# Performance work log

Hardware: AMD Instinct MI355X
Metric: run time of the kernel (lower is better)

Reference implementation:

```python
import jax, jax.numpy as jnp
import numpy as np

B, C, H, W = 8, 3, 64, 64
HORIZON = 32
WIDTH = 32
M1 = M2 = M3 = 8
N_LAYERS = 4
C_OUT = 3


def setup_inputs() -> dict:
    key = jax.random.key(0)
    ks = jax.random.split(key, 16)
    scale = 1.0 / (WIDTH * WIDTH)
    wshape = (N_LAYERS, 4, WIDTH, WIDTH, M1, M2, M3)
    return {
        "x_t": jax.random.normal(ks[0], (B, C, H, W), dtype=jnp.float32),
        "p_w": jax.random.normal(ks[1], (WIDTH, C + 3), dtype=jnp.float32) * 0.1,
        "p_b": jnp.zeros((WIDTH,), dtype=jnp.float32),
        "spec_wr": scale * jax.random.normal(ks[2], wshape, dtype=jnp.float32),
        "spec_wi": scale * jax.random.normal(ks[3], wshape, dtype=jnp.float32),
        "pw_w": jax.random.normal(ks[4], (N_LAYERS, WIDTH, WIDTH), dtype=jnp.float32) * 0.1,
        "pw_b": jnp.zeros((N_LAYERS, WIDTH), dtype=jnp.float32),
        "q1_w": jax.random.normal(ks[5], (2 * WIDTH, WIDTH), dtype=jnp.float32) * 0.1,
        "q1_b": jnp.zeros((2 * WIDTH,), dtype=jnp.float32),
        "q2_w": jax.random.normal(ks[6], (C_OUT, 2 * WIDTH), dtype=jnp.float32) * 0.1,
        "q2_b": jnp.zeros((C_OUT,), dtype=jnp.float32),
        "horizon": HORIZON,
    }


def _conv1x1(x, w, b):
    # x: [b, i, x, y, z], w: [o, i] -> [b, o, x, y, z]
    return jnp.einsum("oi,bixyz->boxyz", w, x) + b[None, :, None, None, None]


def _spectral_conv3d(x, wr, wi):
    # x: [b, i, H, W, T]; wr/wi: [4, i, o, m1, m2, m3]
    h, w_, t = x.shape[-3], x.shape[-2], x.shape[-1]
    xf = jnp.fft.rfftn(x, axes=(-3, -2, -1))  # [b, i, H, W, T//2+1]
    wc = (wr + 1j * wi).astype(xf.dtype)
    m1 = min(M1, xf.shape[-3]); m2 = min(M2, xf.shape[-2]); m3 = min(M3, xf.shape[-1])
    mul = lambda a, ww: jnp.einsum("bixyz,ioxyz->boxyz", a, ww)
    out = jnp.zeros((x.shape[0], wr.shape[2]) + xf.shape[2:], dtype=xf.dtype)
    out = out.at[:, :, :m1, :m2, :m3].set(mul(xf[:, :, :m1, :m2, :m3], wc[0, :, :, :m1, :m2, :m3]))
    out = out.at[:, :, -m1:, :m2, :m3].set(mul(xf[:, :, -m1:, :m2, :m3], wc[1, :, :, :m1, :m2, :m3]))
    out = out.at[:, :, :m1, -m2:, :m3].set(mul(xf[:, :, :m1, -m2:, :m3], wc[2, :, :, :m1, :m2, :m3]))
    out = out.at[:, :, -m1:, -m2:, :m3].set(mul(xf[:, :, -m1:, -m2:, :m3], wc[3, :, :, :m1, :m2, :m3]))
    return jnp.fft.irfftn(out, s=(h, w_, t), axes=(-3, -2, -1))


def _grid_3d(b, h, w, t, dtype):
    gy = jnp.broadcast_to(jnp.linspace(0.0, 1.0, h, dtype=dtype)[None, None, :, None, None], (b, 1, h, w, t))
    gx = jnp.broadcast_to(jnp.linspace(0.0, 1.0, w, dtype=dtype)[None, None, None, :, None], (b, 1, h, w, t))
    gt = jnp.broadcast_to(jnp.linspace(0.0, 1.0, t, dtype=dtype)[None, None, None, None, :], (b, 1, h, w, t))
    return jnp.concatenate([gy, gx, gt], axis=1)


def reference(x_t, p_w, p_b, spec_wr, spec_wi, pw_w, pw_b, q1_w, q1_b, q2_w, q2_b, horizon):
    b, c, h, w = x_t.shape
    x = jnp.broadcast_to(x_t[..., None], (b, c, h, w, horizon))  # repeat over time
    grid = _grid_3d(b, h, w, horizon, x_t.dtype)
    x = jnp.concatenate([x, grid], axis=1)  # [b, c+3, h, w, t]
    x = _conv1x1(x, p_w, p_b)
    for l in range(N_LAYERS):
        x = jax.nn.gelu(
            _spectral_conv3d(x, spec_wr[l], spec_wi[l]) + _conv1x1(x, pw_w[l], pw_b[l]),
            approximate=False,
        )
    x = _conv1x1(x, q1_w, q1_b)
    x = jax.nn.gelu(x, approximate=False)
    x = _conv1x1(x, q2_w, q2_b)
    # [b, c_out, h, w, t] -> [b, t, c_out, h, w]
    return jnp.transpose(x, (0, 4, 1, 2, 3))
```

## Files before the change

### kernel.cpp

```cpp
#include <hip/hip_runtime.h>
#include <math.h>


#define TWO_PI 6.2831853071795864769f

typedef short bf16x8 __attribute__((ext_vector_type(8)));
typedef float f32x4 __attribute__((ext_vector_type(4)));
typedef float v2f __attribute__((ext_vector_type(2)));

__device__ __forceinline__ f32x4 mfma16(bf16x8 a, bf16x8 b, f32x4 c) {
    return __builtin_amdgcn_mfma_f32_16x16x32_bf16(a, b, c, 0, 0, 0);
}

__device__ __forceinline__ void split8(float4 a, float4 b, bf16x8& h, bf16x8& l) {
    float f[8] = {a.x, a.y, a.z, a.w, b.x, b.y, b.z, b.w};
    #pragma unroll
    for (int i = 0; i < 8; ++i) {
        unsigned u = __float_as_uint(f[i]);
        h[i] = (short)(u >> 16);
        float hf = __uint_as_float(u & 0xFFFF0000u);
        float lf = f[i] - hf;
        l[i] = (short)(__float_as_uint(lf) >> 16);
    }
}

__device__ __forceinline__ unsigned packhl(float f) {
    unsigned u = __float_as_uint(f);
    unsigned hi = u & 0xFFFF0000u;
    float lf = f - __uint_as_float(hi);
    return hi | (__float_as_uint(lf) >> 16);
}

__device__ __forceinline__ void unpack8(uint4 a, uint4 b, bf16x8& h, bf16x8& l) {
    unsigned u[8] = {a.x, a.y, a.z, a.w, b.x, b.y, b.z, b.w};
    #pragma unroll
    for (int i = 0; i < 8; ++i) {
        h[i] = (short)(u[i] >> 16);
        l[i] = (short)(u[i] & 0xFFFFu);
    }
}

__device__ __forceinline__ v2f make2(float x) { v2f r; r.x = x; r.y = x; return r; }
__device__ __forceinline__ v2f fma2(v2f a, v2f b, v2f c) { return __builtin_elementwise_fma(a, b, c); }

__device__ __forceinline__ v2f gelu2(v2f v) {
    v2f u = v * 0.70710678118654752f;
    v2f a = __builtin_elementwise_abs(u);
    v2f den = fma2(a, make2(0.3275911f), make2(1.0f));
    v2f t; t.x = __builtin_amdgcn_rcpf(den.x); t.y = __builtin_amdgcn_rcpf(den.y);
    v2f p = t * (0.254829592f + t * (-0.284496736f + t * (1.421413741f +
            t * (-1.453152027f + t * 1.061405429f))));
    v2f e; e.x = __expf(-u.x * u.x); e.y = __expf(-u.y * u.y);
    v2f m = fma2(-p, e, make2(1.0f));
    v2f erfu = __builtin_elementwise_copysign(m, u);
    return 0.5f * v * (1.0f + erfu);
}

__device__ __forceinline__ void gelu4(f32x4& q) {
    v2f p0; p0.x = q[0]; p0.y = q[1];
    v2f p1; p1.x = q[2]; p1.y = q[3];
    p0 = gelu2(p0); p1 = gelu2(p1);
    q[0] = p0.x; q[1] = p0.y; q[2] = p1.x; q[3] = p1.y;
}

__device__ __forceinline__ void make_fwd_A(int l15, int quad, bf16x8& Gh, bf16x8& Gl) {
    int k = l15 >> 1;
    float s0, c0, ds, dc;
    __sincosf((float)(k * quad * 8) * (TWO_PI / 32.0f), &s0, &c0);
    __sincosf((float)k * (TWO_PI / 32.0f), &ds, &dc);
    float m[8];
    float cc = c0, ss = s0;
    #pragma unroll
    for (int j = 0; j < 8; ++j) {
        m[j] = (l15 & 1) ? -ss : cc;
        float nc = cc * dc - ss * ds;
        float ns = ss * dc + cc * ds;
        cc = nc; ss = ns;
    }
    split8(make_float4(m[0], m[1], m[2], m[3]),
           make_float4(m[4], m[5], m[6], m[7]), Gh, Gl);
}

__device__ __forceinline__ void fwd_tdft(const unsigned* up, int b, int sp0,
                                         float2* __restrict__ T1,
                                         int wb, int l15, int quad,
                                         bf16x8 Gh, bf16x8 Gl) {
    #pragma unroll
    for (int nt = 0; nt < 4; ++nt) {
        int r = wb + nt * 16 + l15;
        const uint4* p = (const uint4*)(up + r * 36 + quad * 8);
        bf16x8 bh, bl; unpack8(p[0], p[1], bh, bl);
        f32x4 d = {0.f, 0.f, 0.f, 0.f};
        d = mfma16(Gh, bh, d);
        d = mfma16(Gl, bh, d);
        d = mfma16(Gh, bl, d);
        int c = r & 31, spl = r >> 5;
        float4* ob = (float4*)(T1 + ((long)(b * 32 + c) * 4096 + sp0 + spl) * 8 + quad * 2);
        *ob = make_float4(d[0], d[1], d[2], d[3]);
    }
}

__device__ __forceinline__ void make_invx_A(int x0, int l15, int quad, bf16x8& Ah, bf16x8& Al) {
    int spl = l15 >> 1, ro = l15 & 1;
    float xx = (float)(x0 + spl);
    const float S = 1.0f / 131072.0f;
    float f[8];
    #pragma unroll
    for (int m = 0; m < 4; ++m) {
        int kxi = quad * 4 + m;
        float kx = (float)(kxi < 8 ? kxi : kxi - 16);
        float sn, cs;
        __sincosf(kx * xx * (TWO_PI / 64.0f), &sn, &cs);
        f[2 * m]     = ro ? S * sn : S * cs;
        f[2 * m + 1] = ro ? S * cs : -S * sn;
    }
    split8(make_float4(f[0], f[1], f[2], f[3]),
           make_float4(f[4], f[5], f[6], f[7]), Ah, Al);
}

__device__ __forceinline__ void stage_T5_half(const float2* __restrict__ T5, float* smem,
                                              int b, int y, int half, int tid) {
    float2* T5h = (float2*)(smem + 4224);
    int c = tid >> 4, q4 = tid & 15;
    const float4* src = (const float4*)(T5 + ((long)((b * 32 + half * 16 + c) * 64 + y)) * 128);
    float4* dst = (float4*)(T5h + c * 130);
    #pragma unroll
    for (int j = 0; j < 4; ++j) dst[q4 + j * 16] = src[q4 + j * 16];
}

__device__ __forceinline__ void invx_half(float* smem, int half, int wave, int l15, int quad,
                                          bf16x8 xAh, bf16x8 xAl) {
    const float2* T5h = (const float2*)(smem + 4224);
    #pragma unroll
    for (int nt2 = 0; nt2 < 2; ++nt2) {
        int tile = wave * 2 + nt2;
        int ol = tile * 2 + (l15 >> 3), kt = l15 & 7;
        float f[8];
        #pragma unroll
        for (int m = 0; m < 4; ++m) {
            float2 v = T5h[ol * 130 + (quad * 4 + m) * 8 + kt];
            f[2 * m] = v.x; f[2 * m + 1] = v.y;
        }
        bf16x8 bh, bl;
        split8(make_float4(f[0], f[1], f[2], f[3]),
               make_float4(f[4], f[5], f[6], f[7]), bh, bl);
        f32x4 d = {0.f, 0.f, 0.f, 0.f};
        d = mfma16(xAh, bh, d);
        d = mfma16(xAl, bh, d);
        d = mfma16(xAh, bl, d);
        int o = half * 16 + ol;
        #pragma unroll
        for (int reg = 0; reg < 4; ++reg) {
            int m_ = quad * 4 + reg, spl = m_ >> 1, ri = m_ & 1;
            smem[o * 132 + spl * 16 + kt * 2 + ri] = d[reg];
        }
    }
}

__global__ __launch_bounds__(256) void k_lift(const float* __restrict__ xt,
                                              const float* __restrict__ pw,
                                              const float* __restrict__ pb,
                                              unsigned* __restrict__ X,
                                              float2* __restrict__ T1) {
    __shared__ unsigned xs[9216];
    int gg = blockIdx.x;
    int g = ((gg & 7) << 9) | (gg >> 3);
    int spt = g & 511, b = g >> 9;
    int sp0 = spt * 8;
    int y = sp0 >> 6, x0 = sp0 & 63;
    int tid = threadIdx.x;
    int t = tid & 31, spl = tid >> 5;
    int sp = sp0 + spl;
    float a0 = xt[(b * 3 + 0) * 4096 + sp];
    float a1 = xt[(b * 3 + 1) * 4096 + sp];
    float a2 = xt[(b * 3 + 2) * 4096 + sp];
    float gy = y * (1.0f / 63.0f), gx = (x0 + spl) * (1.0f / 63.0f), gt = t * (1.0f / 31.0f);
    float v[32];
    #pragma unroll
    for (int c = 0; c < 32; ++c) {
        const float* w = pw + c * 6;
        v[c] = pb[c] + w[0] * a0 + w[1] * a1 + w[2] * a2
             + w[3] * gy + w[4] * gx + w[5] * gt;
    }
    unsigned pk[32];
    #pragma unroll
    for (int c = 0; c < 32; ++c) pk[c] = packhl(v[c]);
    unsigned* xg = X + (((long)(b * 4096 + sp)) * 32 + t) * 32;
    #pragma unroll
    for (int j = 0; j < 8; ++j)
        ((uint4*)xg)[j] = make_uint4(pk[4*j], pk[4*j+1], pk[4*j+2], pk[4*j+3]);
    #pragma unroll
    for (int c = 0; c < 32; ++c)
        xs[(spl * 32 + c) * 36 + t] = pk[c];
    int wave = tid >> 6, lane = tid & 63, l15 = lane & 15, quad = lane >> 4;
    bf16x8 Gh, Gl; make_fwd_A(l15, quad, Gh, Gl);
    __syncthreads();
    fwd_tdft(xs, b, sp0, T1, wave * 64, l15, quad, Gh, Gl);
}

__global__ __launch_bounds__(256) void k_xdft(const float2* __restrict__ T1, float2* __restrict__ T2) {
    __shared__ float2 s[1024];
    __shared__ float2 tw[64];
    int g = blockIdx.x;
    int ypair = g & 31; int bc = g >> 5;
    long base = ((long)bc * 64 + ypair * 2) * 512;
    int tid = threadIdx.x;
    for (int k = tid; k < 1024; k += 256) s[k] = T1[base + k];
    if (tid < 64) { float sn, cs; __sincosf(tid * (TWO_PI / 64.0f), &sn, &cs); tw[tid] = make_float2(cs, sn); }
    __syncthreads();
    #pragma unroll
    for (int r = 0; r < 2; ++r) {
        int j = tid + r * 256;
        int half = j >> 8, rem = j & 255;
        int idx = half * 512 + rem;
        float2 a = s[idx], b2 = s[idx + 256];
        s[idx] = make_float2(a.x + b2.x, a.y + b2.y);
        s[idx + 256] = make_float2(a.x - b2.x, a.y - b2.y);
    }
    __syncthreads();
    int half = tid >> 7, jj = tid & 127;
    int kxi = jj >> 3, kt = jj & 7;
    int kx = kxi < 8 ? kxi : kxi + 48;
    const float2* row = s + half * 512 + (kx & 1) * 256;
    float sr = 0.f, si = 0.f;
    for (int x = 0; x < 32; ++x) {
        float2 w = tw[(kx * x) & 63];
        float2 a = row[x * 8 + kt];
        sr += a.x * w.x + a.y * w.y;
        si += a.y * w.x - a.x * w.y;
    }
    T2[((long)bc * 64 + ypair * 2 + half) * 128 + jj] = make_float2(sr, si);
}

__global__ __launch_bounds__(128) void k_ydft(const float2* __restrict__ T2, float2* __restrict__ T3) {
    __shared__ float2 s[512];
    __shared__ float2 tw[64];
    int g = blockIdx.x;
    int kx = g & 15; int bc = g >> 4;
    int tid = threadIdx.x;
    for (int k = tid; k < 512; k += 128) {
        int y = k >> 3, kt = k & 7;
        s[k] = T2[((long)bc * 64 + y) * 128 + kx * 8 + kt];
    }
    if (tid < 64) { float sn, cs; __sincosf(tid * (TWO_PI / 64.0f), &sn, &cs); tw[tid] = make_float2(cs, sn); }
    __syncthreads();
    #pragma unroll
    for (int r = 0; r < 2; ++r) {
        int j = tid + r * 128;
        float2 a = s[j], b2 = s[j + 256];
        s[j] = make_float2(a.x + b2.x, a.y + b2.y);
        s[j + 256] = make_float2(a.x - b2.x, a.y - b2.y);
    }
    __syncthreads();
    int kyi = tid >> 3, kt = tid & 7;
    int ky = kyi < 8 ? kyi : kyi + 48;
    const float2* row = s + (ky & 1) * 256;
    float sr = 0.f, si = 0.f;
    for (int y = 0; y < 32; ++y) {
        float2 w = tw[(ky * y) & 63];
        float2 a = row[y * 8 + kt];
        sr += a.x * w.x + a.y * w.y;
        si += a.y * w.x - a.x * w.y;
    }
    T3[((long)bc * 256 + kyi * 16 + kx) * 8 + kt] = make_float2(sr, si);
}

__global__ __launch_bounds__(256) void k_mix2(const float2* __restrict__ T3,
                                              const float* __restrict__ wr,
                                              const float* __restrict__ wi,
                                              float2* __restrict__ T4, int layer) {
    __shared__ float2 s[2304];
    int mode = blockIdx.x;
    int kyi = mode >> 4, kxi = mode & 15;
    int tid = threadIdx.x;
    {
        int bb = tid >> 5, i = tid & 31;
        const float2* src = T3 + ((long)(bb * 32 + i) * 256 + mode) * 8;
        float2* dst = s + (i * 8 + bb) * 9;
        #pragma unroll
        for (int k = 0; k < 8; ++k) dst[k] = src[k];
    }
    __syncthreads();
    int corner = (kyi >= 8 ? 1 : 0) + (kxi >= 8 ? 2 : 0);
    long wbase = (long)(layer * 4 + corner) * 524288 + (long)(kyi & 7) * 64 + (long)(kxi & 7) * 8;
    int o = tid >> 3, kt = tid & 7;
    long wb = wbase + (long)o * 512 + kt;
    float2 acc[8];
    #pragma unroll
    for (int bb = 0; bb < 8; ++bb) acc[bb] = make_float2(0.f, 0.f);
    for (int i = 0; i < 32; ++i) {
        float r = wr[wb + (long)i * 16384], im = wi[wb + (long)i * 16384];
        #pragma unroll
        for (int bb = 0; bb < 8; ++bb) {
            float2 a = s[(i * 8 + bb) * 9 + kt];
            acc[bb].x += a.x * r - a.y * im;
            acc[bb].y += a.x * im + a.y * r;
        }
    }
    #pragma unroll
    for (int bb = 0; bb < 8; ++bb)
        T4[((long)(bb * 32 + o) * 256 + mode) * 8 + kt] = acc[bb];
}

__global__ __launch_bounds__(256) void k_invy(const float2* __restrict__ T4, float2* __restrict__ T5) {
    __shared__ float2 s[128];
    __shared__ float2 tw[64];
    __shared__ float2 pmP[56], pmM[56];
    int g = blockIdx.x;
    int kx = g & 15; int bc = g >> 4;
    int tid = threadIdx.x;
    if (tid < 128) {
        int kyi = tid >> 3, kt = tid & 7;
        s[tid] = T4[((long)bc * 256 + kyi * 16 + kx) * 8 + kt];
    } else if (tid < 192) {
        int m = tid - 128; float sn, cs; __sincosf(m * (TWO_PI / 64.0f), &sn, &cs); tw[m] = make_float2(cs, sn);
    }
    __syncthreads();
    if (tid < 56) {
        int j = (tid >> 3) + 1, kt = tid & 7;
        float2 a = s[j * 8 + kt], b2 = s[(16 - j) * 8 + kt];
        pmP[tid] = make_float2(a.x + b2.x, a.y + b2.y);
        pmM[tid] = make_float2(a.x - b2.x, a.y - b2.y);
    }
    __syncthreads();
    #pragma unroll
    for (int r = 0; r < 2; ++r) {
        int j = tid + r * 256;
        int y = j >> 3, kt = j & 7;
        float2 A0 = s[kt], A8 = s[64 + kt];
        float2 w8 = tw[(8 * y) & 63];
        float sr = A0.x + A8.x * w8.x + A8.y * w8.y;
        float si = A0.y + A8.y * w8.x - A8.x * w8.y;
        #pragma unroll
        for (int jj = 1; jj < 8; ++jj) {
            float2 w = tw[(jj * y) & 63];
            float2 P = pmP[(jj - 1) * 8 + kt], M = pmM[(jj - 1) * 8 + kt];
            sr += P.x * w.x - M.y * w.y;
            si += P.y * w.x + M.x * w.y;
        }
        T5[((long)bc * 64 + y) * 128 + kx * 8 + kt] = make_float2(sr, si);
    }
}

__device__ __forceinline__ void make_invt_A(int l15, int quad, bf16x8 Ah[2], bf16x8 Al[2]) {
    #pragma unroll
    for (int th = 0; th < 2; ++th) {
        float m[8];
        if (quad < 2) {
            int tt = th * 16 + l15;
            #pragma unroll
            for (int kk = 0; kk < 4; ++kk) {
                int k = quad * 4 + kk;
                float sn, cs;
                __sincosf((float)(k * tt) * (TWO_PI / 32.0f), &sn, &cs);
                float w = k ? 2.0f : 1.0f;
                m[2 * kk] = w * cs;
                m[2 * kk + 1] = -w * sn;
            }
        } else {
            #pragma unroll
            for (int j = 0; j < 8; ++j) m[j] = 0.f;
        }
        split8(make_float4(m[0], m[1], m[2], m[3]),
               make_float4(m[4], m[5], m[6], m[7]), Ah[th], Al[th]);
    }
}

__global__ __launch_bounds__(256) void k_fuse3(unsigned* __restrict__ X, const float2* __restrict__ T5,
                                               const float* __restrict__ pww,
                                               const float* __restrict__ pwb,
                                               float2* __restrict__ T1, int layer) {
    __shared__ float smem[9216];
    int gg = blockIdx.x;
    int g = ((gg & 7) << 9) | (gg >> 3);
    int spt = g & 511, b = g >> 9;
    int sp0 = spt * 8;
    int y = sp0 >> 6, x0 = sp0 & 63;
    int tid = threadIdx.x;
    int wave = tid >> 6, lane = tid & 63, l15 = lane & 15, quad = lane >> 4;
    int wb = wave * 64;
    stage_T5_half(T5, smem, b, y, 0, tid);
    const float* wl = pww + layer * 1024;
    const float* bl = pwb + layer * 32;
    bf16x8 wah[2], wal[2];
    f32x4 acc[2][4];
    #pragma unroll
    for (int mt = 0; mt < 2; ++mt) {
        const float4* p = (const float4*)(wl + (mt * 16 + l15) * 32 + quad * 8);
        split8(p[0], p[1], wah[mt], wal[mt]);
        float4 bv = *(const float4*)(bl + mt * 16 + quad * 4);
        f32x4 bi; bi[0] = bv.x; bi[1] = bv.y; bi[2] = bv.z; bi[3] = bv.w;
        #pragma unroll
        for (int nt = 0; nt < 4; ++nt) acc[mt][nt] = bi;
    }
    #pragma unroll
    for (int nt = 0; nt < 4; ++nt) {
        int pt = wb + nt * 16 + l15;
        int spl = pt >> 5, t = pt & 31;
        const uint4* xp = (const uint4*)(X + (((long)(b * 4096 + sp0 + spl)) * 32 + t) * 32 + quad * 8);
        bf16x8 bh, blo; unpack8(xp[0], xp[1], bh, blo);
        #pragma unroll
        for (int mt = 0; mt < 2; ++mt) {
            acc[mt][nt] = mfma16(wah[mt], bh, acc[mt][nt]);
            acc[mt][nt] = mfma16(wal[mt], bh, acc[mt][nt]);
            acc[mt][nt] = mfma16(wah[mt], blo, acc[mt][nt]);
        }
    }
    bf16x8 Ah[2], Al[2];
    make_invt_A(l15, quad, Ah, Al);
    bf16x8 xAh, xAl;
    make_invx_A(x0, l15, quad, xAh, xAl);
    __syncthreads();
    invx_half(smem, 0, wave, l15, quad, xAh, xAl);
    __syncthreads();
    stage_T5_half(T5, smem, b, y, 1, tid);
    __syncthreads();
    invx_half(smem, 1, wave, l15, quad, xAh, xAl);
    __syncthreads();
    float2* ts = (float2*)smem;
    bf16x8 Bh[2][2], Bl[2][2];
    #pragma unroll
    for (int sph = 0; sph < 2; ++sph) {
        int spl = 2 * wave + sph;
        #pragma unroll
        for (int ch = 0; ch < 2; ++ch) {
            float4 q0 = make_float4(0.f, 0.f, 0.f, 0.f), q1 = q0;
            if (quad < 2) {
                const float4* p = (const float4*)(ts + (ch * 16 + l15) * 66 + spl * 8 + quad * 4);
                q0 = p[0]; q1 = p[1];
            }
            split8(q0, q1, Bh[sph][ch], Bl[sph][ch]);
        }
    }
    __syncthreads();
    #pragma unroll
    for (int sph = 0; sph < 2; ++sph)
        #pragma unroll
        for (int ch = 0; ch < 2; ++ch)
            #pragma unroll
            for (int th = 0; th < 2; ++th) {
                int nt = sph * 2 + th;
                acc[ch][nt] = mfma16(Bh[sph][ch], Ah[th], acc[ch][nt]);
                acc[ch][nt] = mfma16(Bl[sph][ch], Ah[th], acc[ch][nt]);
                acc[ch][nt] = mfma16(Bh[sph][ch], Al[th], acc[ch][nt]);
            }
    bf16x8 Gh, Gl; make_fwd_A(l15, quad, Gh, Gl);
    #pragma unroll
    for (int mt = 0; mt < 2; ++mt)
        #pragma unroll
        for (int nt = 0; nt < 4; ++nt) gelu4(acc[mt][nt]);
    unsigned* up = (unsigned*)smem;
    #pragma unroll
    for (int mt = 0; mt < 2; ++mt)
        #pragma unroll
        for (int nt = 0; nt < 4; ++nt) {
            int pt = wb + nt * 16 + l15;
            int spl = pt >> 5, t = pt & 31;
            int o0 = mt * 16 + quad * 4;
            unsigned pk0 = packhl(acc[mt][nt][0]), pk1 = packhl(acc[mt][nt][1]);
            unsigned pk2 = packhl(acc[mt][nt][2]), pk3 = packhl(acc[mt][nt][3]);
            *(uint4*)(X + (((long)(b * 4096 + sp0 + spl)) * 32 + t) * 32 + o0) =
                make_uint4(pk0, pk1, pk2, pk3);
            up[(spl * 32 + o0 + 0) * 36 + t] = pk0;
            up[(spl * 32 + o0 + 1) * 36 + t] = pk1;
            up[(spl * 32 + o0 + 2) * 36 + t] = pk2;
            up[(spl * 32 + o0 + 3) * 36 + t] = pk3;
        }
    __syncthreads();
    fwd_tdft(up, b, sp0, T1, wb, l15, quad, Gh, Gl);
}

__global__ __launch_bounds__(256) void k_fuse3_last(const unsigned* __restrict__ X, const float2* __restrict__ T5,
                                                    const float* __restrict__ pww, const float* __restrict__ pwb,
                                                    const float* __restrict__ q1w, const float* __restrict__ q1b,
                                                    const float* __restrict__ q2w, const float* __restrict__ q2b,
                                                    float* __restrict__ out) {
    __shared__ float smem[9408];
    int gg = blockIdx.x;
    int g = ((gg & 7) << 9) | (gg >> 3);
    int spt = g & 511, b = g >> 9;
    int sp0 = spt * 8;
    int y = sp0 >> 6, x0 = sp0 & 63;
    int tid = threadIdx.x;
    int wave = tid >> 6, lane = tid & 63, l15 = lane & 15, quad = lane >> 4;
    int wb = wave * 64;
    stage_T5_half(T5, smem, b, y, 0, tid);
    if (tid < 192) smem[9216 + tid] = q2w[tid];
    const float* wl = pww + 3 * 1024;
    const float* bl = pwb + 3 * 32;
    bf16x8 wah[2], wal[2];
    f32x4 acc[2][4];
    #pragma unroll
    for (int mt = 0; mt < 2; ++mt) {
        const float4* p = (const float4*)(wl + (mt * 16 + l15) * 32 + quad * 8);
        split8(p[0], p[1], wah[mt], wal[mt]);
        float4 bv = *(const float4*)(bl + mt * 16 + quad * 4);
        f32x4 bi; bi[0] = bv.x; bi[1] = bv.y; bi[2] = bv.z; bi[3] = bv.w;
        #pragma unroll
        for (int nt = 0; nt < 4; ++nt) acc[mt][nt] = bi;
    }
    #pragma unroll
    for (int nt = 0; nt < 4; ++nt) {
        int pt = wb + nt * 16 + l15;
        int spl = pt >> 5, t = pt & 31;
        const uint4* xp = (const uint4*)(X + (((long)(b * 4096 + sp0 + spl)) * 32 + t) * 32 + quad * 8);
        bf16x8 bh, blo; unpack8(xp[0], xp[1], bh, blo);
        #pragma unroll
        for (int mt = 0; mt < 2; ++mt) {
            acc[mt][nt] = mfma16(wah[mt], bh, acc[mt][nt]);
            acc[mt][nt] = mfma16(wal[mt], bh, acc[mt][nt]);
            acc[mt][nt] = mfma16(wah[mt], blo, acc[mt][nt]);
        }
    }
    bf16x8 Ah[2], Al[2];
    make_invt_A(l15, quad, Ah, Al);
    bf16x8 xAh, xAl;
    make_invx_A(x0, l15, quad, xAh, xAl);
    __syncthreads();
    invx_half(smem, 0, wave, l15, quad, xAh, xAl);
    __syncthreads();
    stage_T5_half(T5, smem, b, y, 1, tid);
    __syncthreads();
    invx_half(smem, 1, wave, l15, quad, xAh, xAl);
    __syncthreads();
    float2* ts = (float2*)smem;
    bf16x8 Bh[2][2], Bl[2][2];
    #pragma unroll
    for (int sph = 0; sph < 2; ++sph) {
        int spl = 2 * wave + sph;
        #pragma unroll
        for (int ch = 0; ch < 2; ++ch) {
            float4 q0 = make_float4(0.f, 0.f, 0.f, 0.f), q1 = q0;
            if (quad < 2) {
                const float4* p = (const float4*)(ts + (ch * 16 + l15) * 66 + spl * 8 + quad * 4);
                q0 = p[0]; q1 = p[1];
            }
            split8(q0, q1, Bh[sph][ch], Bl[sph][ch]);
        }
    }
    __syncthreads();
    #pragma unroll
    for (int sph = 0; sph < 2; ++sph)
        #pragma unroll
        for (int ch = 0; ch < 2; ++ch)
            #pragma unroll
            for (int th = 0; th < 2; ++th) {
                int nt = sph * 2 + th;
                acc[ch][nt] = mfma16(Bh[sph][ch], Ah[th], acc[ch][nt]);
                acc[ch][nt] = mfma16(Bl[sph][ch], Ah[th], acc[ch][nt]);
                acc[ch][nt] = mfma16(Bh[sph][ch], Al[th], acc[ch][nt]);
            }
    #pragma unroll
    for (int mt = 0; mt < 2; ++mt)
        #pragma unroll
        for (int nt = 0; nt < 4; ++nt) gelu4(acc[mt][nt]);
    unsigned* up = (unsigned*)smem;
    #pragma unroll
    for (int mt = 0; mt < 2; ++mt)
        #pragma unroll
        for (int nt = 0; nt < 4; ++nt) {
            int pt = wb + nt * 16 + l15;
            int o0 = mt * 16 + quad * 4;
            *(uint4*)(up + pt * 36 + o0) =
                make_uint4(packhl(acc[mt][nt][0]), packhl(acc[mt][nt][1]),
                           packhl(acc[mt][nt][2]), packhl(acc[mt][nt][3]));
        }
    __syncthreads();
    bf16x8 qah[4], qal[4];
    f32x4 qbv[4];
    #pragma unroll
    for (int mt = 0; mt < 4; ++mt) {
        const float4* p = (const float4*)(q1w + (mt * 16 + l15) * 32 + quad * 8);
        split8(p[0], p[1], qah[mt], qal[mt]);
        float4 bv = *(const float4*)(q1b + mt * 16 + quad * 4);
        qbv[mt][0] = bv.x; qbv[mt][1] = bv.y; qbv[mt][2] = bv.z; qbv[mt][3] = bv.w;
    }
    const float* q2l = smem + 9216;
    float q2b0 = q2b[0], q2b1 = q2b[1], q2b2 = q2b[2];
    float oc0[4], oc1[4], oc2[4];
    #pragma unroll
    for (int nt = 0; nt < 4; ++nt) {
        int pt = wb + nt * 16 + l15;
        const uint4* bp = (const uint4*)(up + pt * 36 + quad * 8);
        bf16x8 bh, blo; unpack8(bp[0], bp[1], bh, blo);
        float p0 = 0.f, p1 = 0.f, p2 = 0.f;
        #pragma unroll
        for (int mt = 0; mt < 4; ++mt) {
            f32x4 h = qbv[mt];
            h = mfma16(qah[mt], bh, h);
            h = mfma16(qal[mt], bh, h);
            h = mfma16(qah[mt], blo, h);
            gelu4(h);
            #pragma unroll
            for (int reg = 0; reg < 4; ++reg) {
                int hh = mt * 16 + quad * 4 + reg;
                p0 += q2l[hh] * h[reg];
                p1 += q2l[64 + hh] * h[reg];
                p2 += q2l[128 + hh] * h[reg];
            }
        }
        p0 += __shfl_xor(p0, 16); p0 += __shfl_xor(p0, 32);
        p1 += __shfl_xor(p1, 16); p1 += __shfl_xor(p1, 32);
        p2 += __shfl_xor(p2, 16); p2 += __shfl_xor(p2, 32);
        oc0[nt] = p0 + q2b0; oc1[nt] = p1 + q2b1; oc2[nt] = p2 + q2b2;
    }
    __syncthreads();
    if (quad == 0) {
        #pragma unroll
        for (int nt = 0; nt < 4; ++nt) {
            int pt = wb + nt * 16 + l15;
            int spl = pt >> 5, t = pt & 31;
            smem[(t * 3 + 0) * 9 + spl] = oc0[nt];
            smem[(t * 3 + 1) * 9 + spl] = oc1[nt];
            smem[(t * 3 + 2) * 9 + spl] = oc2[nt];
        }
    }
    __syncthreads();
    for (int m = tid; m < 768; m += 256) {
        int u = m >> 3, spl = m & 7;
        out[((long)(b * 96 + u)) * 4096 + sp0 + spl] = smem[u * 9 + spl];
    }
}

extern "C" void kernel_launch(void* const* d_in, const int* in_sizes, int n_in,
                              void* d_out, int out_size, void* d_ws, size_t ws_size,
                              hipStream_t stream) {
    const float* xt  = (const float*)d_in[0];
    const float* pw  = (const float*)d_in[1];
    const float* pb  = (const float*)d_in[2];
    const float* swr = (const float*)d_in[3];
    const float* swi = (const float*)d_in[4];
    const float* pww = (const float*)d_in[5];
    const float* pwb = (const float*)d_in[6];
    const float* q1w = (const float*)d_in[7];
    const float* q1b = (const float*)d_in[8];
    const float* q2w = (const float*)d_in[9];
    const float* q2b = (const float*)d_in[10];
    float* out = (float*)d_out;

    unsigned* X  = (unsigned*)d_ws;
    float2* T1 = (float2*)((float*)d_ws + 33554432);
    float2* T2 = (float2*)((float*)T1 + 16777216);
    float2* T3 = (float2*)((float*)T2 + 4194304);
    float2* T4 = (float2*)((float*)T3 + 1048576);

    k_lift<<<4096, 256, 0, stream>>>(xt, pw, pb, X, T1);
    for (int l = 0; l < 4; ++l) {
        k_xdft<<<8192, 256, 0, stream>>>(T1, T2);
        k_ydft<<<4096, 128, 0, stream>>>(T2, T3);
        k_mix2<<<256, 256, 0, stream>>>(T3, swr, swi, T4, l);
        k_invy<<<4096, 256, 0, stream>>>(T4, T2);
        if (l < 3)
            k_fuse3<<<4096, 256, 0, stream>>>(X, T2, pww, pwb, T1, l);
        else
            k_fuse3_last<<<4096, 256, 0, stream>>>(X, T2, pww, pwb, q1w, q1b, q2w, q2b, out);
    }
}
```

Before: 720.7 us.

## Precompute DFT fragment tables once, store packed bf16 splits in LDS, mix in place

Adds a one-block init kernel that builds the inverse-time, forward-time and inverse-x DFT matrix fragments (pre-split into bf16 hi/lo) into a workspace table. The lift and fuse kernels then load these instead of recomputing them with sincos per block. The inverse-x result is also written to LDS already packed as hi/lo bf16, so the later read only unpacks it and skips a second split. k_mix2 appears to write its output back into T3 instead of a separate T4, dropping one buffer. The cost is an extra launch plus global table loads, and the in-place mix is only safe if each block reads its own slice before writing.

Measured after the change: 762.9 us. +5.9%, slower.

```diff
diff --git a/kernel.cpp b/kernel.cpp
--- a/kernel.cpp
+++ b/kernel.cpp
@@ -81,25 +81,6 @@
            make_float4(m[4], m[5], m[6], m[7]), Gh, Gl);
 }
 
-__device__ __forceinline__ void fwd_tdft(const unsigned* up, int b, int sp0,
-                                         float2* __restrict__ T1,
-                                         int wb, int l15, int quad,
-                                         bf16x8 Gh, bf16x8 Gl) {
-    #pragma unroll
-    for (int nt = 0; nt < 4; ++nt) {
-        int r = wb + nt * 16 + l15;
-        const uint4* p = (const uint4*)(up + r * 36 + quad * 8);
-        bf16x8 bh, bl; unpack8(p[0], p[1], bh, bl);
-        f32x4 d = {0.f, 0.f, 0.f, 0.f};
-        d = mfma16(Gh, bh, d);
-        d = mfma16(Gl, bh, d);
-        d = mfma16(Gh, bl, d);
-        int c = r & 31, spl = r >> 5;
-        float4* ob = (float4*)(T1 + ((long)(b * 32 + c) * 4096 + sp0 + spl) * 8 + quad * 2);
-        *ob = make_float4(d[0], d[1], d[2], d[3]);
-    }
-}
-
 __device__ __forceinline__ void make_invx_A(int x0, int l15, int quad, bf16x8& Ah, bf16x8& Al) {
     int spl = l15 >> 1, ro = l15 & 1;
     float xx = (float)(x0 + spl);
@@ -116,230 +97,6 @@
     }
     split8(make_float4(f[0], f[1], f[2], f[3]),
            make_float4(f[4], f[5], f[6], f[7]), Ah, Al);
-}
-
-__device__ __forceinline__ void stage_T5_half(const float2* __restrict__ T5, float* smem,
-                                              int b, int y, int half, int tid) {
-    float2* T5h = (float2*)(smem + 4224);
-    int c = tid >> 4, q4 = tid & 15;
-    const float4* src = (const float4*)(T5 + ((long)((b * 32 + half * 16 + c) * 64 + y)) * 128);
-    float4* dst = (float4*)(T5h + c * 130);
-    #pragma unroll
-    for (int j = 0; j < 4; ++j) dst[q4 + j * 16] = src[q4 + j * 16];
-}
-
-__device__ __forceinline__ void invx_half(float* smem, int half, int wave, int l15, int quad,
-                                          bf16x8 xAh, bf16x8 xAl) {
-    const float2* T5h = (const float2*)(smem + 4224);
-    #pragma unroll
-    for (int nt2 = 0; nt2 < 2; ++nt2) {
-        int tile = wave * 2 + nt2;
-        int ol = tile * 2 + (l15 >> 3), kt = l15 & 7;
-        float f[8];
-        #pragma unroll
-        for (int m = 0; m < 4; ++m) {
-            float2 v = T5h[ol * 130 + (quad * 4 + m) * 8 + kt];
-            f[2 * m] = v.x; f[2 * m + 1] = v.y;
-        }
-        bf16x8 bh, bl;
-        split8(make_float4(f[0], f[1], f[2], f[3]),
-               make_float4(f[4], f[5], f[6], f[7]), bh, bl);
-        f32x4 d = {0.f, 0.f, 0.f, 0.f};
-        d = mfma16(xAh, bh, d);
-        d = mfma16(xAl, bh, d);
-        d = mfma16(xAh, bl, d);
-        int o = half * 16 + ol;
-        #pragma unroll
-        for (int reg = 0; reg < 4; ++reg) {
-            int m_ = quad * 4 + reg, spl = m_ >> 1, ri = m_ & 1;
-            smem[o * 132 + spl * 16 + kt * 2 + ri] = d[reg];
-        }
-    }
-}
-
-__global__ __launch_bounds__(256) void k_lift(const float* __restrict__ xt,
-                                              const float* __restrict__ pw,
-                                              const float* __restrict__ pb,
-                                              unsigned* __restrict__ X,
-                                              float2* __restrict__ T1) {
-    __shared__ unsigned xs[9216];
-    int gg = blockIdx.x;
-    int g = ((gg & 7) << 9) | (gg >> 3);
-    int spt = g & 511, b = g >> 9;
-    int sp0 = spt * 8;
-    int y = sp0 >> 6, x0 = sp0 & 63;
-    int tid = threadIdx.x;
-    int t = tid & 31, spl = tid >> 5;
-    int sp = sp0 + spl;
-    float a0 = xt[(b * 3 + 0) * 4096 + sp];
-    float a1 = xt[(b * 3 + 1) * 4096 + sp];
-    float a2 = xt[(b * 3 + 2) * 4096 + sp];
-    float gy = y * (1.0f / 63.0f), gx = (x0 + spl) * (1.0f / 63.0f), gt = t * (1.0f / 31.0f);
-    float v[32];
-    #pragma unroll
-    for (int c = 0; c < 32; ++c) {
-        const float* w = pw + c * 6;
-        v[c] = pb[c] + w[0] * a0 + w[1] * a1 + w[2] * a2
-             + w[3] * gy + w[4] * gx + w[5] * gt;
-    }
-    unsigned pk[32];
-    #pragma unroll
-    for (int c = 0; c < 32; ++c) pk[c] = packhl(v[c]);
-    unsigned* xg = X + (((long)(b * 4096 + sp)) * 32 + t) * 32;
-    #pragma unroll
-    for (int j = 0; j < 8; ++j)
-        ((uint4*)xg)[j] = make_uint4(pk[4*j], pk[4*j+1], pk[4*j+2], pk[4*j+3]);
-    #pragma unroll
-    for (int c = 0; c < 32; ++c)
-        xs[(spl * 32 + c) * 36 + t] = pk[c];
-    int wave = tid >> 6, lane = tid & 63, l15 = lane & 15, quad = lane >> 4;
-    bf16x8 Gh, Gl; make_fwd_A(l15, quad, Gh, Gl);
-    __syncthreads();
-    fwd_tdft(xs, b, sp0, T1, wave * 64, l15, quad, Gh, Gl);
-}
-
-__global__ __launch_bounds__(256) void k_xdft(const float2* __restrict__ T1, float2* __restrict__ T2) {
-    __shared__ float2 s[1024];
-    __shared__ float2 tw[64];
-    int g = blockIdx.x;
-    int ypair = g & 31; int bc = g >> 5;
-    long base = ((long)bc * 64 + ypair * 2) * 512;
-    int tid = threadIdx.x;
-    for (int k = tid; k < 1024; k += 256) s[k] = T1[base + k];
-    if (tid < 64) { float sn, cs; __sincosf(tid * (TWO_PI / 64.0f), &sn, &cs); tw[tid] = make_float2(cs, sn); }
-    __syncthreads();
-    #pragma unroll
-    for (int r = 0; r < 2; ++r) {
-        int j = tid + r * 256;
-        int half = j >> 8, rem = j & 255;
-        int idx = half * 512 + rem;
-        float2 a = s[idx], b2 = s[idx + 256];
-        s[idx] = make_float2(a.x + b2.x, a.y + b2.y);
-        s[idx + 256] = make_float2(a.x - b2.x, a.y - b2.y);
-    }
-    __syncthreads();
-    int half = tid >> 7, jj = tid & 127;
-    int kxi = jj >> 3, kt = jj & 7;
-    int kx = kxi < 8 ? kxi : kxi + 48;
-    const float2* row = s + half * 512 + (kx & 1) * 256;
-    float sr = 0.f, si = 0.f;
-    for (int x = 0; x < 32; ++x) {
-        float2 w = tw[(kx * x) & 63];
-        float2 a = row[x * 8 + kt];
-        sr += a.x * w.x + a.y * w.y;
-        si += a.y * w.x - a.x * w.y;
-    }
-    T2[((long)bc * 64 + ypair * 2 + half) * 128 + jj] = make_float2(sr, si);
-}
-
-__global__ __launch_bounds__(128) void k_ydft(const float2* __restrict__ T2, float2* __restrict__ T3) {
-    __shared__ float2 s[512];
-    __shared__ float2 tw[64];
-    int g = blockIdx.x;
-    int kx = g & 15; int bc = g >> 4;
-    int tid = threadIdx.x;
-    for (int k = tid; k < 512; k += 128) {
-        int y = k >> 3, kt = k & 7;
-        s[k] = T2[((long)bc * 64 + y) * 128 + kx * 8 + kt];
-    }
-    if (tid < 64) { float sn, cs; __sincosf(tid * (TWO_PI / 64.0f), &sn, &cs); tw[tid] = make_float2(cs, sn); }
-    __syncthreads();
-    #pragma unroll
-    for (int r = 0; r < 2; ++r) {
-        int j = tid + r * 128;
-        float2 a = s[j], b2 = s[j + 256];
-        s[j] = make_float2(a.x + b2.x, a.y + b2.y);
-        s[j + 256] = make_float2(a.x - b2.x, a.y - b2.y);
-    }
-    __syncthreads();
-    int kyi = tid >> 3, kt = tid & 7;
-    int ky = kyi < 8 ? kyi : kyi + 48;
-    const float2* row = s + (ky & 1) * 256;
-    float sr = 0.f, si = 0.f;
-    for (int y = 0; y < 32; ++y) {
-        float2 w = tw[(ky * y) & 63];
-        float2 a = row[y * 8 + kt];
-        sr += a.x * w.x + a.y * w.y;
-        si += a.y * w.x - a.x * w.y;
-    }
-    T3[((long)bc * 256 + kyi * 16 + kx) * 8 + kt] = make_float2(sr, si);
-}
-
-__global__ __launch_bounds__(256) void k_mix2(const float2* __restrict__ T3,
-                                              const float* __restrict__ wr,
-                                              const float* __restrict__ wi,
-                                              float2* __restrict__ T4, int layer) {
-    __shared__ float2 s[2304];
-    int mode = blockIdx.x;
-    int kyi = mode >> 4, kxi = mode & 15;
-    int tid = threadIdx.x;
-    {
-        int bb = tid >> 5, i = tid & 31;
-        const float2* src = T3 + ((long)(bb * 32 + i) * 256 + mode) * 8;
-        float2* dst = s + (i * 8 + bb) * 9;
-        #pragma unroll
-        for (int k = 0; k < 8; ++k) dst[k] = src[k];
-    }
-    __syncthreads();
-    int corner = (kyi >= 8 ? 1 : 0) + (kxi >= 8 ? 2 : 0);
-    long wbase = (long)(layer * 4 + corner) * 524288 + (long)(kyi & 7) * 64 + (long)(kxi & 7) * 8;
-    int o = tid >> 3, kt = tid & 7;
-    long wb = wbase + (long)o * 512 + kt;
-    float2 acc[8];
-    #pragma unroll
-    for (int bb = 0; bb < 8; ++bb) acc[bb] = make_float2(0.f, 0.f);
-    for (int i = 0; i < 32; ++i) {
-        float r = wr[wb + (long)i * 16384], im = wi[wb + (long)i * 16384];
-        #pragma unroll
-        for (int bb = 0; bb < 8; ++bb) {
-            float2 a = s[(i * 8 + bb) * 9 + kt];
-            acc[bb].x += a.x * r - a.y * im;
-            acc[bb].y += a.x * im + a.y * r;
-        }
-    }
-    #pragma unroll
-    for (int bb = 0; bb < 8; ++bb)
-        T4[((long)(bb * 32 + o) * 256 + mode) * 8 + kt] = acc[bb];
-}
-
-__global__ __launch_bounds__(256) void k_invy(const float2* __restrict__ T4, float2* __restrict__ T5) {
-    __shared__ float2 s[128];
-    __shared__ float2 tw[64];
-    __shared__ float2 pmP[56], pmM[56];
-    int g = blockIdx.x;
-    int kx = g & 15; int bc = g >> 4;
-    int tid = threadIdx.x;
-    if (tid < 128) {
-        int kyi = tid >> 3, kt = tid & 7;
-        s[tid] = T4[((long)bc * 256 + kyi * 16 + kx) * 8 + kt];
-    } else if (tid < 192) {
-        int m = tid - 128; float sn, cs; __sincosf(m * (TWO_PI / 64.0f), &sn, &cs); tw[m] = make_float2(cs, sn);
-    }
-    __syncthreads();
-    if (tid < 56) {
-        int j = (tid >> 3) + 1, kt = tid & 7;
-        float2 a = s[j * 8 + kt], b2 = s[(16 - j) * 8 + kt];
-        pmP[tid] = make_float2(a.x + b2.x, a.y + b2.y);
-        pmM[tid] = make_float2(a.x - b2.x, a.y - b2.y);
-    }
-    __syncthreads();
-    #pragma unroll
-    for (int r = 0; r < 2; ++r) {
-        int j = tid + r * 256;
-        int y = j >> 3, kt = j & 7;
-        float2 A0 = s[kt], A8 = s[64 + kt];
-        float2 w8 = tw[(8 * y) & 63];
-        float sr = A0.x + A8.x * w8.x + A8.y * w8.y;
-        float si = A0.y + A8.y * w8.x - A8.x * w8.y;
-        #pragma unroll
-        for (int jj = 1; jj < 8; ++jj) {
-            float2 w = tw[(jj * y) & 63];
-            float2 P = pmP[(jj - 1) * 8 + kt], M = pmM[(jj - 1) * 8 + kt];
-            sr += P.x * w.x - M.y * w.y;
-            si += P.y * w.x + M.x * w.y;
-        }
-        T5[((long)bc * 64 + y) * 128 + kx * 8 + kt] = make_float2(sr, si);
-    }
 }
 
 __device__ __forceinline__ void make_invt_A(int l15, int quad, bf16x8 Ah[2], bf16x8 Al[2]) {
@@ -366,10 +123,296 @@
     }
 }
 
+__device__ __forceinline__ unsigned packfrag(short h, short l) {
+    return ((unsigned)(unsigned short)h << 16) | (unsigned)(unsigned short)l;
+}
+
+__global__ __launch_bounds__(512) void k_init(unsigned* __restrict__ tabs) {
+    int tid = threadIdx.x;
+    int lane = tid & 63, xg = tid >> 6;
+    int l15 = lane & 15, quad = lane >> 4;
+    if (tid < 64) {
+        bf16x8 Ah[2], Al[2];
+        make_invt_A(l15, quad, Ah, Al);
+        #pragma unroll
+        for (int th = 0; th < 2; ++th)
+            #pragma unroll
+            for (int i = 0; i < 8; ++i)
+                tabs[lane * 16 + th * 8 + i] = packfrag(Ah[th][i], Al[th][i]);
+        bf16x8 Gh, Gl;
+        make_fwd_A(l15, quad, Gh, Gl);
+        #pragma unroll
+        for (int i = 0; i < 8; ++i)
+            tabs[1024 + lane * 8 + i] = packfrag(Gh[i], Gl[i]);
+    }
+    bf16x8 xAh, xAl;
+    make_invx_A(xg * 8, l15, quad, xAh, xAl);
+    #pragma unroll
+    for (int i = 0; i < 8; ++i)
+        tabs[1536 + xg * 512 + lane * 8 + i] = packfrag(xAh[i], xAl[i]);
+}
+
+__device__ __forceinline__ void load_invt(const uint4* tb, int lane, bf16x8 Ah[2], bf16x8 Al[2]) {
+    unpack8(tb[lane * 4 + 0], tb[lane * 4 + 1], Ah[0], Al[0]);
+    unpack8(tb[lane * 4 + 2], tb[lane * 4 + 3], Ah[1], Al[1]);
+}
+__device__ __forceinline__ void load_fwd(const uint4* tb, int lane, bf16x8& Gh, bf16x8& Gl) {
+    unpack8(tb[256 + lane * 2], tb[256 + lane * 2 + 1], Gh, Gl);
+}
+__device__ __forceinline__ void load_invx(const uint4* tb, int xg, int lane, bf16x8& Ah, bf16x8& Al) {
+    unpack8(tb[384 + (xg * 64 + lane) * 2], tb[384 + (xg * 64 + lane) * 2 + 1], Ah, Al);
+}
+
+__device__ __forceinline__ void fwd_tdft(const unsigned* up, int b, int sp0,
+                                         float2* __restrict__ T1,
+                                         int wb, int l15, int quad,
+                                         bf16x8 Gh, bf16x8 Gl) {
+    #pragma unroll
+    for (int nt = 0; nt < 4; ++nt) {
+        int r = wb + nt * 16 + l15;
+        const uint4* p = (const uint4*)(up + r * 36 + quad * 8);
+        bf16x8 bh, bl; unpack8(p[0], p[1], bh, bl);
+        f32x4 d = {0.f, 0.f, 0.f, 0.f};
+        d = mfma16(Gh, bh, d);
+        d = mfma16(Gl, bh, d);
+        d = mfma16(Gh, bl, d);
+        int c = r & 31, spl = r >> 5;
+        float4* ob = (float4*)(T1 + ((long)(b * 32 + c) * 4096 + sp0 + spl) * 8 + quad * 2);
+        *ob = make_float4(d[0], d[1], d[2], d[3]);
+    }
+}
+
+__device__ __forceinline__ void stage_T5_half(const float2* __restrict__ T5, float* smem,
+                                              int b, int y, int half, int tid) {
+    float2* T5h = (float2*)(smem + 4224);
+    int c = tid >> 4, q4 = tid & 15;
+    const float4* src = (const float4*)(T5 + ((long)((b * 32 + half * 16 + c) * 64 + y)) * 128);
+    float4* dst = (float4*)(T5h + c * 130);
+    #pragma unroll
+    for (int j = 0; j < 4; ++j) dst[q4 + j * 16] = src[q4 + j * 16];
+}
+
+__device__ __forceinline__ void invx_half(float* smem, int half, int wave, int l15, int quad,
+                                          bf16x8 xAh, bf16x8 xAl) {
+    const float2* T5h = (const float2*)(smem + 4224);
+    unsigned* tsu = (unsigned*)smem;
+    #pragma unroll
+    for (int nt2 = 0; nt2 < 2; ++nt2) {
+        int tile = wave * 2 + nt2;
+        int ol = tile * 2 + (l15 >> 3), kt = l15 & 7;
+        float f[8];
+        #pragma unroll
+        for (int m = 0; m < 4; ++m) {
+            float2 v = T5h[ol * 130 + (quad * 4 + m) * 8 + kt];
+            f[2 * m] = v.x; f[2 * m + 1] = v.y;
+        }
+        bf16x8 bh, bl;
+        split8(make_float4(f[0], f[1], f[2], f[3]),
+               make_float4(f[4], f[5], f[6], f[7]), bh, bl);
+        f32x4 d = {0.f, 0.f, 0.f, 0.f};
+        d = mfma16(xAh, bh, d);
+        d = mfma16(xAl, bh, d);
+        d = mfma16(xAh, bl, d);
+        int o = half * 16 + ol;
+        #pragma unroll
+        for (int reg = 0; reg < 4; ++reg) {
+            int m_ = quad * 4 + reg, spl = m_ >> 1, ri = m_ & 1;
+            tsu[o * 132 + spl * 16 + kt * 2 + ri] = packhl(d[reg]);
+        }
+    }
+}
+
+__global__ __launch_bounds__(256) void k_lift(const float* __restrict__ xt,
+                                              const float* __restrict__ pw,
+                                              const float* __restrict__ pb,
+                                              unsigned* __restrict__ X,
+                                              float2* __restrict__ T1,
+                                              const unsigned* __restrict__ tabs) {
+    __shared__ unsigned xs[9216];
+    int gg = blockIdx.x;
+    int g = ((gg & 7) << 9) | (gg >> 3);
+    int spt = g & 511, b = g >> 9;
+    int sp0 = spt * 8;
+    int y = sp0 >> 6, x0 = sp0 & 63;
+    int tid = threadIdx.x;
+    int t = tid & 31, spl = tid >> 5;
+    int sp = sp0 + spl;
+    float a0 = xt[(b * 3 + 0) * 4096 + sp];
+    float a1 = xt[(b * 3 + 1) * 4096 + sp];
+    float a2 = xt[(b * 3 + 2) * 4096 + sp];
+    float gy = y * (1.0f / 63.0f), gx = (x0 + spl) * (1.0f / 63.0f), gt = t * (1.0f / 31.0f);
+    float v[32];
+    #pragma unroll
+    for (int c = 0; c < 32; ++c) {
+        const float* w = pw + c * 6;
+        v[c] = pb[c] + w[0] * a0 + w[1] * a1 + w[2] * a2
+             + w[3] * gy + w[4] * gx + w[5] * gt;
+    }
+    unsigned pk[32];
+    #pragma unroll
+    for (int c = 0; c < 32; ++c) pk[c] = packhl(v[c]);
+    unsigned* xg2 = X + (((long)(b * 4096 + sp)) * 32 + t) * 32;
+    #pragma unroll
+    for (int j = 0; j < 8; ++j)
+        ((uint4*)xg2)[j] = make_uint4(pk[4*j], pk[4*j+1], pk[4*j+2], pk[4*j+3]);
+    #pragma unroll
+    for (int c = 0; c < 32; ++c)
+        xs[(spl * 32 + c) * 36 + t] = pk[c];
+    int wave = tid >> 6, lane = tid & 63, l15 = lane & 15, quad = lane >> 4;
+    bf16x8 Gh, Gl; load_fwd((const uint4*)tabs, lane, Gh, Gl);
+    __syncthreads();
+    fwd_tdft(xs, b, sp0, T1, wave * 64, l15, quad, Gh, Gl);
+}
+
+__global__ __launch_bounds__(256) void k_xdft(const float2* __restrict__ T1, float2* __restrict__ T2) {
+    __shared__ float2 s[1024];
+    __shared__ float2 tw[64];
+    int g = blockIdx.x;
+    int ypair = g & 31; int bc = g >> 5;
+    long base = ((long)bc * 64 + ypair * 2) * 512;
+    int tid = threadIdx.x;
+    for (int k = tid; k < 1024; k += 256) s[k] = T1[base + k];
+    if (tid < 64) { float sn, cs; __sincosf(tid * (TWO_PI / 64.0f), &sn, &cs); tw[tid] = make_float2(cs, sn); }
+    __syncthreads();
+    #pragma unroll
+    for (int r = 0; r < 2; ++r) {
+        int j = tid + r * 256;
+        int half = j >> 8, rem = j & 255;
+        int idx = half * 512 + rem;
+        float2 a = s[idx], b2 = s[idx + 256];
+        s[idx] = make_float2(a.x + b2.x, a.y + b2.y);
+        s[idx + 256] = make_float2(a.x - b2.x, a.y - b2.y);
+    }
+    __syncthreads();
+    int half = tid >> 7, jj = tid & 127;
+    int kxi = jj >> 3, kt = jj & 7;
+    int kx = kxi < 8 ? kxi : kxi + 48;
+    const float2* row = s + half * 512 + (kx & 1) * 256;
+    float sr = 0.f, si = 0.f;
+    for (int x = 0; x < 32; ++x) {
+        float2 w = tw[(kx * x) & 63];
+        float2 a = row[x * 8 + kt];
+        sr += a.x * w.x + a.y * w.y;
+        si += a.y * w.x - a.x * w.y;
+    }
+    T2[((long)bc * 64 + ypair * 2 + half) * 128 + jj] = make_float2(sr, si);
+}
+
+__global__ __launch_bounds__(128) void k_ydft(const float2* __restrict__ T2, float2* __restrict__ T3) {
+    __shared__ float2 s[512];
+    __shared__ float2 tw[64];
+    int g = blockIdx.x;
+    int kx = g & 15; int bc = g >> 4;
+    int tid = threadIdx.x;
+    for (int k = tid; k < 512; k += 128) {
+        int y = k >> 3, kt = k & 7;
+        s[k] = T2[((long)bc * 64 + y) * 128 + kx * 8 + kt];
+    }
+    if (tid < 64) { float sn, cs; __sincosf(tid * (TWO_PI / 64.0f), &sn, &cs); tw[tid] = make_float2(cs, sn); }
+    __syncthreads();
+    #pragma unroll
+    for (int r = 0; r < 2; ++r) {
+        int j = tid + r * 128;
+        float2 a = s[j], b2 = s[j + 256];
+        s[j] = make_float2(a.x + b2.x, a.y + b2.y);
+        s[j + 256] = make_float2(a.x - b2.x, a.y - b2.y);
+    }
+    __syncthreads();
+    int kyi = tid >> 3, kt = tid & 7;
+    int ky = kyi < 8 ? kyi : kyi + 48;
+    const float2* row = s + (ky & 1) * 256;
+    float sr = 0.f, si = 0.f;
+    for (int y = 0; y < 32; ++y) {
+        float2 w = tw[(ky * y) & 63];
+        float2 a = row[y * 8 + kt];
+        sr += a.x * w.x + a.y * w.y;
+        si += a.y * w.x - a.x * w.y;
+    }
+    T3[((long)bc * 256 + kyi * 16 + kx) * 8 + kt] = make_float2(sr, si);
+}
+
+__global__ __launch_bounds__(256) void k_mix2(float2* __restrict__ T3,
+                                              const float* __restrict__ wr,
+                                              const float* __restrict__ wi,
+                                              int layer) {
+    __shared__ float2 s[2304];
+    int mode = blockIdx.x;
+    int kyi = mode >> 4, kxi = mode & 15;
+    int tid = threadIdx.x;
+    {
+        int bb = tid >> 5, i = tid & 31;
+        const float2* src = T3 + ((long)(bb * 32 + i) * 256 + mode) * 8;
+        float2* dst = s + (i * 8 + bb) * 9;
+        #pragma unroll
+        for (int k = 0; k < 8; ++k) dst[k] = src[k];
+    }
+    __syncthreads();
+    int corner = (kyi >= 8 ? 1 : 0) + (kxi >= 8 ? 2 : 0);
+    long wbase = (long)(layer * 4 + corner) * 524288 + (long)(kyi & 7) * 64 + (long)(kxi & 7) * 8;
+    int o = tid >> 3, kt = tid & 7;
+    long wb = wbase + (long)o * 512 + kt;
+    float2 acc[8];
+    #pragma unroll
+    for (int bb = 0; bb < 8; ++bb) acc[bb] = make_float2(0.f, 0.f);
+    for (int i = 0; i < 32; ++i) {
+        float r = wr[wb + (long)i * 16384], im = wi[wb + (long)i * 16384];
+        #pragma unroll
+        for (int bb = 0; bb < 8; ++bb) {
+            float2 a = s[(i * 8 + bb) * 9 + kt];
+            acc[bb].x += a.x * r - a.y * im;
+            acc[bb].y += a.x * im + a.y * r;
+        }
+    }
+    #pragma unroll
+    for (int bb = 0; bb < 8; ++bb)
+        T3[((long)(bb * 32 + o) * 256 + mode) * 8 + kt] = acc[bb];
+}
+
+__global__ __launch_bounds__(256) void k_invy(const float2* __restrict__ T4, float2* __restrict__ T5) {
+    __shared__ float2 s[128];
+    __shared__ float2 tw[64];
+    __shared__ float2 pmP[56], pmM[56];
+    int g = blockIdx.x;
+    int kx = g & 15; int bc = g >> 4;
+    int tid = threadIdx.x;
+    if (tid < 128) {
+        int kyi = tid >> 3, kt = tid & 7;
+        s[tid] = T4[((long)bc * 256 + kyi * 16 + kx) * 8 + kt];
+    } else if (tid < 192) {
+        int m = tid - 128; float sn, cs; __sincosf(m * (TWO_PI / 64.0f), &sn, &cs); tw[m] = make_float2(cs, sn);
+    }
+    __syncthreads();
+    if (tid < 56) {
+        int j = (tid >> 3) + 1, kt = tid & 7;
+        float2 a = s[j * 8 + kt], b2 = s[(16 - j) * 8 + kt];
+        pmP[tid] = make_float2(a.x + b2.x, a.y + b2.y);
+        pmM[tid] = make_float2(a.x - b2.x, a.y - b2.y);
+    }
+    __syncthreads();
+    #pragma unroll
+    for (int r = 0; r < 2; ++r) {
+        int j = tid + r * 256;
+        int y = j >> 3, kt = j & 7;
+        float2 A0 = s[kt], A8 = s[64 + kt];
+        float2 w8 = tw[(8 * y) & 63];
+        float sr = A0.x + A8.x * w8.x + A8.y * w8.y;
+        float si = A0.y + A8.y * w8.x - A8.x * w8.y;
+        #pragma unroll
+        for (int jj = 1; jj < 8; ++jj) {
+            float2 w = tw[(jj * y) & 63];
+            float2 P = pmP[(jj - 1) * 8 + kt], M = pmM[(jj - 1) * 8 + kt];
+            sr += P.x * w.x - M.y * w.y;
+            si += P.y * w.x + M.x * w.y;
+        }
+        T5[((long)bc * 64 + y) * 128 + kx * 8 + kt] = make_float2(sr, si);
+    }
+}
+
 __global__ __launch_bounds__(256) void k_fuse3(unsigned* __restrict__ X, const float2* __restrict__ T5,
                                                const float* __restrict__ pww,
                                                const float* __restrict__ pwb,
-                                               float2* __restrict__ T1, int layer) {
+                                               float2* __restrict__ T1, int layer,
+                                               const unsigned* __restrict__ tabs) {
     __shared__ float smem[9216];
     int gg = blockIdx.x;
     int g = ((gg & 7) << 9) | (gg >> 3);
@@ -379,6 +422,7 @@
     int tid = threadIdx.x;
     int wave = tid >> 6, lane = tid & 63, l15 = lane & 15, quad = lane >> 4;
     int wb = wave * 64;
+    const uint4* tb = (const uint4*)tabs;
     stage_T5_half(T5, smem, b, y, 0, tid);
     const float* wl = pww + layer * 1024;
     const float* bl = pwb + layer * 32;
@@ -407,9 +451,9 @@
         }
     }
     bf16x8 Ah[2], Al[2];
-    make_invt_A(l15, quad, Ah, Al);
+    load_invt(tb, lane, Ah, Al);
     bf16x8 xAh, xAl;
-    make_invx_A(x0, l15, quad, xAh, xAl);
+    load_invx(tb, x0 >> 3, lane, xAh, xAl);
     __syncthreads();
     invx_half(smem, 0, wave, l15, quad, xAh, xAl);
     __syncthreads();
@@ -417,19 +461,19 @@
     __syncthreads();
     invx_half(smem, 1, wave, l15, quad, xAh, xAl);
     __syncthreads();
-    float2* ts = (float2*)smem;
+    const unsigned* tsu = (const unsigned*)smem;
     bf16x8 Bh[2][2], Bl[2][2];
     #pragma unroll
     for (int sph = 0; sph < 2; ++sph) {
         int spl = 2 * wave + sph;
         #pragma unroll
         for (int ch = 0; ch < 2; ++ch) {
-            float4 q0 = make_float4(0.f, 0.f, 0.f, 0.f), q1 = q0;
+            uint4 q0 = make_uint4(0, 0, 0, 0), q1 = q0;
             if (quad < 2) {
-                const float4* p = (const float4*)(ts + (ch * 16 + l15) * 66 + spl * 8 + quad * 4);
+                const uint4* p = (const uint4*)(tsu + (ch * 16 + l15) * 132 + spl * 16 + quad * 8);
                 q0 = p[0]; q1 = p[1];
             }
-            split8(q0, q1, Bh[sph][ch], Bl[sph][ch]);
+            unpack8(q0, q1, Bh[sph][ch], Bl[sph][ch]);
         }
     }
     __syncthreads();
@@ -444,7 +488,7 @@
                 acc[ch][nt] = mfma16(Bl[sph][ch], Ah[th], acc[ch][nt]);
                 acc[ch][nt] = mfma16(Bh[sph][ch], Al[th], acc[ch][nt]);
             }
-    bf16x8 Gh, Gl; make_fwd_A(l15, quad, Gh, Gl);
+    bf16x8 Gh, Gl; load_fwd(tb, lane, Gh, Gl);
     #pragma unroll
     for (int mt = 0; mt < 2; ++mt)
         #pragma unroll
@@ -474,7 +518,8 @@
                                                     const float* __restrict__ pww, const float* __restrict__ pwb,
                                                     const float* __restrict__ q1w, const float* __restrict__ q1b,
                                                     const float* __restrict__ q2w, const float* __restrict__ q2b,
-                                                    float* __restrict__ out) {
+                                                    float* __restrict__ out,
+                                                    const unsigned* __restrict__ tabs) {
     __shared__ float smem[9408];
     int gg = blockIdx.x;
     int g = ((gg & 7) << 9) | (gg >> 3);
@@ -484,6 +529,7 @@
     int tid = threadIdx.x;
     int wave = tid >> 6, lane = tid & 63, l15 = lane & 15, quad = lane >> 4;
     int wb = wave * 64;
+    const uint4* tb = (const uint4*)tabs;
     stage_T5_half(T5, smem, b, y, 0, tid);
     if (tid < 192) smem[9216 + tid] = q2w[tid];
     const float* wl = pww + 3 * 1024;
@@ -513,9 +559,9 @@
         }
     }
     bf16x8 Ah[2], Al[2];
-    make_invt_A(l15, quad, Ah, Al);
+    load_invt(tb, lane, Ah, Al);
     bf16x8 xAh, xAl;
-    make_invx_A(x0, l15, quad, xAh, xAl);
+    load_invx(tb, x0 >> 3, lane, xAh, xAl);
     __syncthreads();
     invx_half(smem, 0, wave, l15, quad, xAh, xAl);
     __syncthreads();
@@ -523,19 +569,19 @@
     __syncthreads();
     invx_half(smem, 1, wave, l15, quad, xAh, xAl);
     __syncthreads();
-    float2* ts = (float2*)smem;
+    const unsigned* tsu = (const unsigned*)smem;
     bf16x8 Bh[2][2], Bl[2][2];
     #pragma unroll
     for (int sph = 0; sph < 2; ++sph) {
         int spl = 2 * wave + sph;
         #pragma unroll
         for (int ch = 0; ch < 2; ++ch) {
-            float4 q0 = make_float4(0.f, 0.f, 0.f, 0.f), q1 = q0;
+            uint4 q0 = make_uint4(0, 0, 0, 0), q1 = q0;
             if (quad < 2) {
-                const float4* p = (const float4*)(ts + (ch * 16 + l15) * 66 + spl * 8 + quad * 4);
+                const uint4* p = (const uint4*)(tsu + (ch * 16 + l15) * 132 + spl * 16 + quad * 8);
                 q0 = p[0]; q1 = p[1];
             }
-            split8(q0, q1, Bh[sph][ch], Bl[sph][ch]);
+            unpack8(q0, q1, Bh[sph][ch], Bl[sph][ch]);
         }
     }
     __syncthreads();
@@ -642,17 +688,18 @@
     float2* T1 = (float2*)((float*)d_ws + 33554432);
     float2* T2 = (float2*)((float*)T1 + 16777216);
     float2* T3 = (float2*)((float*)T2 + 4194304);
-    float2* T4 = (float2*)((float*)T3 + 1048576);
-
-    k_lift<<<4096, 256, 0, stream>>>(xt, pw, pb, X, T1);
+    unsigned* tabs = (unsigned*)((float*)T3 + 1048576);
+
+    k_init<<<1, 512, 0, stream>>>(tabs);
+    k_lift<<<4096, 256, 0, stream>>>(xt, pw, pb, X, T1, tabs);
     for (int l = 0; l < 4; ++l) {
         k_xdft<<<8192, 256, 0, stream>>>(T1, T2);
         k_ydft<<<4096, 128, 0, stream>>>(T2, T3);
-        k_mix2<<<256, 256, 0, stream>>>(T3, swr, swi, T4, l);
-        k_invy<<<4096, 256, 0, stream>>>(T4, T2);
+        k_mix2<<<256, 256, 0, stream>>>(T3, swr, swi, l);
+        k_invy<<<4096, 256, 0, stream>>>(T3, T2);
         if (l < 3)
-            k_fuse3<<<4096, 256, 0, stream>>>(X, T2, pww, pwb, T1, l);
+            k_fuse3<<<4096, 256, 0, stream>>>(X, T2, pww, pwb, T1, l, tabs);
         else
-            k_fuse3_last<<<4096, 256, 0, stream>>>(X, T2, pww, pwb, q1w, q1b, q2w, q2b, out);
-    }
-}
+            k_fuse3_last<<<4096, 256, 0, stream>>>(X, T2, pww, pwb, q1w, q1b, q2w, q2b, out, tabs);
+    }
+}
```
